# Kernel optimization log

Measured on AMD Instinct MI355X. Metric: run time of the kernel, lower is better.

## Reference

```python
import jax, jax.numpy as jnp
import numpy as np

NUM_RELATION = 7

def setup_inputs() -> dict:
    key = jax.random.key(0)
    ks = jax.random.split(key, 12)
    N, E, D, DO, R, DE = 20000, 640000, 512, 512, NUM_RELATION, 59
    inp = {
        "node_feat": jax.random.normal(ks[0], (N, D), dtype=jnp.float32),
        "edge_weight": jax.random.uniform(ks[1], (E,), dtype=jnp.float32),
        "edge_feat": jax.random.normal(ks[2], (E, DE), dtype=jnp.float32),
        "W_lin": jax.random.normal(ks[3], (DO, R * D), dtype=jnp.float32) * 0.02,
        "b_lin": jax.random.normal(ks[4], (DO,), dtype=jnp.float32) * 0.02,
        "W_self": jax.random.normal(ks[5], (DO, D), dtype=jnp.float32) * 0.02,
        "b_self": jax.random.normal(ks[6], (DO,), dtype=jnp.float32) * 0.02,
        "W_edge": jax.random.normal(ks[7], (DO, DE), dtype=jnp.float32) * 0.02,
        "b_edge": jax.random.normal(ks[8], (DO,), dtype=jnp.float32) * 0.02,
        "node_in": jax.random.randint(ks[9], (E,), 0, N, dtype=jnp.int64) if jax.config.jax_enable_x64 else jax.random.randint(ks[9], (E,), 0, N).astype(jnp.int32),
        "node_out": jax.random.randint(ks[10], (E,), 0, N).astype(jnp.int32),
        "relation": jax.random.randint(ks[11], (E,), 0, R).astype(jnp.int32),
    }
    inp["node_in"] = inp["node_in"].astype(jnp.int32)
    return inp


def reference(node_feat, edge_weight, edge_feat, W_lin, b_lin, W_self, b_self,
              W_edge, b_edge, node_in, node_out, relation):
    N, D = node_feat.shape
    R = NUM_RELATION
    # segment id: node_out * R + relation  (column index in sparse (N, N*R) adjacency)
    seg = node_out * R + relation  # [E]
    # update = adjacency.T @ input  == scatter-add of weighted source features
    msg = node_feat[node_in] * edge_weight[:, None]               # [E, D]
    update = jax.ops.segment_sum(msg, seg, num_segments=N * R)    # [N*R, D]
    # edge_linear path: edge_update scattered with the same segment ids
    edge_msg = (edge_feat @ W_edge.T + b_edge) * edge_weight[:, None]  # [E, D]
    update = update + jax.ops.segment_sum(edge_msg, seg, num_segments=N * R)
    update = update.reshape(N, R * D)                             # [N, R*D]
    # combine: linear(update) + self_loop(input), then relu
    out = update @ W_lin.T + b_lin + node_feat @ W_self.T + b_self
    return jax.nn.relu(out)
```

## Files before the change

kernel.cpp:

```cpp
#include <hip/hip_runtime.h>
#include <stdint.h>

typedef unsigned short u16;
typedef __attribute__((ext_vector_type(8))) __bf16 bf16x8;
typedef __attribute__((ext_vector_type(8))) unsigned short u16x8;
typedef __attribute__((ext_vector_type(4))) float f32x4;

#define NREL 7
#define DIM  512
#define DEDGE 59
#define KC   420
#define KCP  448
#define KTOT 4544

__device__ __forceinline__ float bf2f(u16 u) {
  union { unsigned u; float f; } c; c.u = ((unsigned)u) << 16; return c.f;
}
__device__ __forceinline__ u16 f2bf(float f) {
  union { float f; unsigned u; } c; c.f = f;
  unsigned r = ((c.u >> 16) & 1u) + 0x7FFFu;
  return (u16)((c.u + r) >> 16);
}

__device__ __forceinline__ void gload16(const void* g, void* l) {
  __builtin_amdgcn_global_load_lds(
      (__attribute__((address_space(1))) void*)g,
      (__attribute__((address_space(3))) void*)l, 16, 0, 0);
}

__global__ void convA(const float* __restrict__ in, u16* __restrict__ out, int total4) {
  int i = blockIdx.x * 256 + threadIdx.x;
  if (i >= total4) return;
  float4 v = ((const float4*)in)[i];
  ushort4 r;
  r.x = f2bf(v.x); r.y = f2bf(v.y); r.z = f2bf(v.z); r.w = f2bf(v.w);
  ((ushort4*)out)[i] = r;
}

__global__ void buildBW(const float* __restrict__ W_lin, const float* __restrict__ W_self,
                        u16* __restrict__ Bfull, int total4) {
  int gid = blockIdx.x * 256 + threadIdx.x;
  if (gid >= total4) return;
  int idx = gid * 4;
  int o = idx >> 12;
  int k = idx & 4095;
  const float* src = (k < NREL * DIM) ? (W_lin + (size_t)o * (NREL * DIM) + k)
                                      : (W_self + (size_t)o * DIM + (k - NREL * DIM));
  float4 v = *(const float4*)src;
  ushort4 rr;
  rr.x = f2bf(v.x); rr.y = f2bf(v.y); rr.z = f2bf(v.z); rr.w = f2bf(v.w);
  *(ushort4*)(Bfull + (size_t)o * KTOT + k) = rr;
}

__global__ __launch_bounds__(512) void buildCx(const float* __restrict__ W_edge,
                                               const float* __restrict__ b_edge,
                                               const float* __restrict__ W_lin,
                                               u16* __restrict__ Bfull) {
  int c = blockIdx.x;
  int o = threadIdx.x;
  u16* dst = Bfull + (size_t)o * KTOT + NREL * DIM + DIM;
  if (c >= KC) { dst[c] = 0; return; }
  __shared__ float col[DIM];
  int r;
  if (c < NREL * DEDGE) {
    r = c / DEDGE;
    int de = c - r * DEDGE;
    col[o] = W_edge[(size_t)o * DEDGE + de];
  } else {
    r = c - NREL * DEDGE;
    col[o] = b_edge[o];
  }
  __syncthreads();
  const float* wrow = W_lin + (size_t)o * (NREL * DIM) + (size_t)r * DIM;
  float acc = 0.f;
#pragma unroll 8
  for (int d = 0; d < DIM; ++d) acc += col[d] * wrow[d];
  dst[c] = f2bf(acc);
}

__global__ void countK2(const int* __restrict__ node_out, const int* __restrict__ relation,
                        int* __restrict__ counts2, int E) {
  int e = blockIdx.x * 256 + threadIdx.x;
  if (e < E) atomicAdd(&counts2[node_out[e] * 8 + relation[e]], 1);
}

__global__ void baseK(const int* __restrict__ counts2, int* __restrict__ offs2,
                      int* __restrict__ cursor2, int* __restrict__ totalCtr, int N) {
  int n = blockIdx.x * 256 + threadIdx.x;
  if (n >= N) return;
  int cnt[NREL];
  int s = 0;
#pragma unroll
  for (int r = 0; r < NREL; ++r) { cnt[r] = counts2[n * 8 + r]; s += cnt[r]; }
  int base = atomicAdd(totalCtr, s);
#pragma unroll
  for (int r = 0; r < NREL; ++r) {
    offs2[n * 8 + r] = base;
    cursor2[n * 8 + r] = base;
    base += cnt[r];
  }
  offs2[n * 8 + 7] = base;
}

__global__ void fillK2(const int* __restrict__ node_in, const int* __restrict__ node_out,
                       const int* __restrict__ relation, const float* __restrict__ ew,
                       int* __restrict__ cursor2, uint4* __restrict__ quads, int E) {
  int e = blockIdx.x * 256 + threadIdx.x;
  if (e >= E) return;
  int p = atomicAdd(&cursor2[node_out[e] * 8 + relation[e]], 1);
  quads[p] = make_uint4((unsigned)node_in[e], __float_as_uint(ew[e]), (unsigned)e, 0u);
}

__global__ __launch_bounds__(64) void gatherG2(const float* __restrict__ ef,
                                               const uint4* __restrict__ quads,
                                               const int* __restrict__ offs2,
                                               u16* __restrict__ Mfull) {
  int n = blockIdx.x;
  int lane = threadIdx.x;
  u16* row = Mfull + (size_t)n * KTOT + NREL * DIM + DIM;
  int base = n * 8;
  for (int r = 0; r < NREL; ++r) {
    int p0 = offs2[base + r], p1 = offs2[base + r + 1];
    float acc = 0.f;
    for (int p = p0; p < p1; ++p) {
      uint4 q = quads[p];
      int e = __builtin_amdgcn_readfirstlane((int)q.z);
      float w = __uint_as_float(__builtin_amdgcn_readfirstlane(q.y));
      float v = (lane < DEDGE) ? ef[(size_t)e * DEDGE + lane] : 1.0f;
      acc += w * v;
    }
    if (lane < DEDGE) row[r * DEDGE + lane] = f2bf(acc);
    else if (lane == DEDGE) row[NREL * DEDGE + r] = f2bf(acc);
  }
  if (lane >= 60) {
    for (int c = KC + (lane - 60); c < KCP; c += 4) row[c] = 0;
  }
}

__global__ __launch_bounds__(256) void aggK(const u16* __restrict__ NF,
                                            const uint4* __restrict__ quads,
                                            const int* __restrict__ offs2,
                                            u16* __restrict__ Mfull) {
  int n = blockIdx.x;
  int wid = threadIdx.x >> 6, lane = threadIdx.x & 63;
  int o0 = lane * 8;
  u16* mrow = Mfull + (size_t)n * KTOT;
  if (wid == 3) {
    *(u16x8*)(mrow + NREL * DIM + o0) = *(const u16x8*)(NF + (size_t)n * DIM + o0);
  }
  int base = n * 8;
  for (int r = wid; r < NREL; r += 4) {
    int p0 = offs2[base + r], p1 = offs2[base + r + 1];
    float a[8];
#pragma unroll
    for (int j = 0; j < 8; ++j) a[j] = 0.f;
    for (int p = p0; p < p1; ++p) {
      uint4 q = quads[p];
      int src = __builtin_amdgcn_readfirstlane((int)q.x);
      float w = __uint_as_float(__builtin_amdgcn_readfirstlane(q.y));
      u16x8 hv = *(const u16x8*)(NF + (size_t)src * DIM + o0);
#pragma unroll
      for (int j = 0; j < 8; ++j) a[j] += w * bf2f(hv[j]);
    }
    u16x8 st;
#pragma unroll
    for (int j = 0; j < 8; ++j) st[j] = f2bf(a[j]);
    *(u16x8*)(mrow + r * DIM + o0) = st;
  }
}

__global__ __launch_bounds__(256) void gemm_br(const u16* __restrict__ A,
                                               const u16* __restrict__ Bt,
                                               const float* __restrict__ b_lin,
                                               const float* __restrict__ b_self,
                                               float* __restrict__ Cout, int M) {
  __shared__ __align__(16) u16 sA[3][128 * 32];
  __shared__ __align__(16) u16 sB[3][128 * 32];
  const int tid = threadIdx.x;
  const int w = tid >> 6, l = tid & 63;
  const int lr = l & 15, kg = l >> 4;
  const int sl = kg ^ ((lr >> 1) & 3);

  const int id = blockIdx.x;
  const int npan = gridDim.x >> 2;
  const int nfull = (npan >> 3) << 3;
  int p, c;
  if (id < nfull * 4) {
    int g = id >> 5, r = id & 31;
    p = g * 8 + (r & 7);
    c = r >> 3;
  } else {
    int t = id - nfull * 4;
    p = nfull + (t >> 2);
    c = t & 3;
  }
  const int m0 = p * 128, n0 = c * 128;
  const int wr = w >> 1, wc = w & 1;
  f32x4 acc[4][4];
  const f32x4 z4 = {0.f, 0.f, 0.f, 0.f};
#pragma unroll
  for (int i = 0; i < 4; ++i)
#pragma unroll
    for (int j = 0; j < 4; ++j) acc[i][j] = z4;

  const int ktiles = KTOT / 32;

  auto stage = [&](int kt, int b) {
    const int k0 = kt * 32;
#pragma unroll
    for (int t = 0; t < 2; ++t) {
      int idx = w * 128 + t * 64 + l;
      int row = idx >> 2, kp = idx & 3;
      int s = kp ^ ((row >> 1) & 3);
      int gm = m0 + row; gm = gm < M ? gm : M - 1;
      gload16(A + (size_t)gm * KTOT + k0 + s * 8,
              (char*)sA[b] + (size_t)idx * 16);
    }
#pragma unroll
    for (int t = 0; t < 2; ++t) {
      int idx = w * 128 + t * 64 + l;
      int row = idx >> 2, kp = idx & 3;
      int s = kp ^ ((row >> 1) & 3);
      gload16(Bt + (size_t)(n0 + row) * KTOT + k0 + s * 8,
              (char*)sB[b] + (size_t)idx * 16);
    }
  };

  stage(0, 0);
  stage(1, 1);
  asm volatile("s_waitcnt vmcnt(4)" ::: "memory");
  __builtin_amdgcn_s_barrier();
  __builtin_amdgcn_sched_barrier(0);

  for (int kt = 0; kt < ktiles; ++kt) {
    const int cur = kt % 3;
    if (kt + 2 < ktiles) stage(kt + 2, (kt + 2) % 3);
    bf16x8 af[4], bfr[4];
#pragma unroll
    for (int i = 0; i < 4; ++i)
      af[i] = *(const bf16x8*)(sA[cur] + (size_t)(wr * 64 + i * 16 + lr) * 32 + sl * 8);
#pragma unroll
    for (int j = 0; j < 4; ++j)
      bfr[j] = *(const bf16x8*)(sB[cur] + (size_t)(wc * 64 + j * 16 + lr) * 32 + sl * 8);
#pragma unroll
    for (int i = 0; i < 4; ++i)
#pragma unroll
      for (int j = 0; j < 4; ++j)
        acc[i][j] = __builtin_amdgcn_mfma_f32_16x16x32_bf16(af[i], bfr[j], acc[i][j], 0, 0, 0);
    if (kt + 2 < ktiles) {
      asm volatile("s_waitcnt vmcnt(4)" ::: "memory");
    } else {
      asm volatile("s_waitcnt vmcnt(0)" ::: "memory");
    }
    __builtin_amdgcn_s_barrier();
    __builtin_amdgcn_sched_barrier(0);
  }
#pragma unroll
  for (int i = 0; i < 4; ++i) {
#pragma unroll
    for (int j = 0; j < 4; ++j) {
      int gj = n0 + wc * 64 + j * 16 + lr;
      float bias = b_lin[gj] + b_self[gj];
#pragma unroll
      for (int v = 0; v < 4; ++v) {
        int gm = m0 + wr * 64 + i * 16 + kg * 4 + v;
        if (gm < M)
          ((float*)Cout)[(size_t)gm * DIM + gj] = fmaxf(acc[i][j][v] + bias, 0.f);
      }
    }
  }
}

extern "C" void kernel_launch(void* const* d_in, const int* in_sizes, int n_in,
                              void* d_out, int out_size, void* d_ws, size_t ws_size,
                              hipStream_t stream) {
  const float* node_feat = (const float*)d_in[0];
  const float* edge_weight = (const float*)d_in[1];
  const float* edge_feat = (const float*)d_in[2];
  const float* W_lin = (const float*)d_in[3];
  const float* b_lin = (const float*)d_in[4];
  const float* W_self = (const float*)d_in[5];
  const float* b_self = (const float*)d_in[6];
  const float* W_edge = (const float*)d_in[7];
  const float* b_edge = (const float*)d_in[8];
  const int* node_in = (const int*)d_in[9];
  const int* node_out = (const int*)d_in[10];
  const int* relation = (const int*)d_in[11];
  float* out = (float*)d_out;

  const int N = in_sizes[0] / DIM;
  const int E = in_sizes[1];

  char* ws = (char*)d_ws;
  size_t off = 0;
  auto take = [&](size_t b) {
    char* p = ws + off;
    off += (b + 255) & ~(size_t)255;
    return p;
  };
  u16* NF       = (u16*)take((size_t)N * DIM * 2);
  u16* Bfull    = (u16*)take((size_t)DIM * KTOT * 2);
  u16* Mfull    = (u16*)take((size_t)N * KTOT * 2);
  int* counts2  = (int*)take((size_t)N * 8 * 4);
  int* offs2    = (int*)take((size_t)N * 8 * 4);
  int* cursor2  = (int*)take((size_t)N * 8 * 4);
  int* totalCtr = (int*)take(256);
  uint4* quads  = (uint4*)take((size_t)E * 16);
  if (off > ws_size) return;

  hipMemsetAsync(counts2, 0, (size_t)N * 8 * 4, stream);
  hipMemsetAsync(totalCtr, 0, 256, stream);

  {
    int total4 = N * DIM / 4;
    convA<<<(total4 + 255) / 256, 256, 0, stream>>>(node_feat, NF, total4);
  }
  {
    int total4 = DIM * 4096 / 4;
    buildBW<<<(total4 + 255) / 256, 256, 0, stream>>>(W_lin, W_self, Bfull, total4);
  }
  buildCx<<<KCP, 512, 0, stream>>>(W_edge, b_edge, W_lin, Bfull);

  countK2<<<(E + 255) / 256, 256, 0, stream>>>(node_out, relation, counts2, E);
  baseK<<<(N + 255) / 256, 256, 0, stream>>>(counts2, offs2, cursor2, totalCtr, N);
  fillK2<<<(E + 255) / 256, 256, 0, stream>>>(node_in, node_out, relation, edge_weight,
                                              cursor2, quads, E);

  gatherG2<<<N, 64, 0, stream>>>(edge_feat, quads, offs2, Mfull);
  aggK<<<N, 256, 0, stream>>>(NF, quads, offs2, Mfull);

  {
    int npan = (N + 127) / 128;
    gemm_br<<<npan * 4, 256, 0, stream>>>(Mfull, Bfull, b_lin, b_self, out, N);
  }
}
```

Baseline: 490.3 us.

## Fuse edge-feature gather into node aggregation and split GEMM A operand buffers

Folds the separate edge-feature gather kernel into the aggregation kernel, so each wave walks the edge list once and accumulates both node-feature and edge-feature sums. It also stops copying node_feat into a combined A matrix: the GEMM now selects among three source buffers (U, NF, G) per k-tile. A one-ahead prefetch of the next edge quad is added to the inner loop. This removes one kernel launch, a second pass over the edge indices, and the self-feature copy, at the cost of extra per-lane loads and a branch in the GEMM staging.

```diff
diff --git a/kernel.cpp b/kernel.cpp
--- a/kernel.cpp
+++ b/kernel.cpp
@@ -11,6 +11,7 @@
 #define DEDGE 59
 #define KC   420
 #define KCP  448
+#define KU   3584
 #define KTOT 4544
 
 __device__ __forceinline__ float bf2f(u16 u) {
@@ -44,8 +45,8 @@
   int idx = gid * 4;
   int o = idx >> 12;
   int k = idx & 4095;
-  const float* src = (k < NREL * DIM) ? (W_lin + (size_t)o * (NREL * DIM) + k)
-                                      : (W_self + (size_t)o * DIM + (k - NREL * DIM));
+  const float* src = (k < KU) ? (W_lin + (size_t)o * KU + k)
+                              : (W_self + (size_t)o * DIM + (k - KU));
   float4 v = *(const float4*)src;
   ushort4 rr;
   rr.x = f2bf(v.x); rr.y = f2bf(v.y); rr.z = f2bf(v.z); rr.w = f2bf(v.w);
@@ -58,7 +59,7 @@
                                                u16* __restrict__ Bfull) {
   int c = blockIdx.x;
   int o = threadIdx.x;
-  u16* dst = Bfull + (size_t)o * KTOT + NREL * DIM + DIM;
+  u16* dst = Bfull + (size_t)o * KTOT + KU + DIM;
   if (c >= KC) { dst[c] = 0; return; }
   __shared__ float col[DIM];
   int r;
@@ -71,7 +72,7 @@
     col[o] = b_edge[o];
   }
   __syncthreads();
-  const float* wrow = W_lin + (size_t)o * (NREL * DIM) + (size_t)r * DIM;
+  const float* wrow = W_lin + (size_t)o * KU + (size_t)r * DIM;
   float acc = 0.f;
 #pragma unroll 8
   for (int d = 0; d < DIM; ++d) acc += col[d] * wrow[d];
@@ -111,65 +112,52 @@
   quads[p] = make_uint4((unsigned)node_in[e], __float_as_uint(ew[e]), (unsigned)e, 0u);
 }
 
-__global__ __launch_bounds__(64) void gatherG2(const float* __restrict__ ef,
-                                               const uint4* __restrict__ quads,
-                                               const int* __restrict__ offs2,
-                                               u16* __restrict__ Mfull) {
-  int n = blockIdx.x;
-  int lane = threadIdx.x;
-  u16* row = Mfull + (size_t)n * KTOT + NREL * DIM + DIM;
-  int base = n * 8;
-  for (int r = 0; r < NREL; ++r) {
-    int p0 = offs2[base + r], p1 = offs2[base + r + 1];
-    float acc = 0.f;
-    for (int p = p0; p < p1; ++p) {
-      uint4 q = quads[p];
-      int e = __builtin_amdgcn_readfirstlane((int)q.z);
-      float w = __uint_as_float(__builtin_amdgcn_readfirstlane(q.y));
-      float v = (lane < DEDGE) ? ef[(size_t)e * DEDGE + lane] : 1.0f;
-      acc += w * v;
-    }
-    if (lane < DEDGE) row[r * DEDGE + lane] = f2bf(acc);
-    else if (lane == DEDGE) row[NREL * DEDGE + r] = f2bf(acc);
-  }
-  if (lane >= 60) {
-    for (int c = KC + (lane - 60); c < KCP; c += 4) row[c] = 0;
-  }
-}
-
 __global__ __launch_bounds__(256) void aggK(const u16* __restrict__ NF,
+                                            const float* __restrict__ ef,
                                             const uint4* __restrict__ quads,
                                             const int* __restrict__ offs2,
-                                            u16* __restrict__ Mfull) {
+                                            u16* __restrict__ U,
+                                            u16* __restrict__ G) {
   int n = blockIdx.x;
   int wid = threadIdx.x >> 6, lane = threadIdx.x & 63;
   int o0 = lane * 8;
-  u16* mrow = Mfull + (size_t)n * KTOT;
-  if (wid == 3) {
-    *(u16x8*)(mrow + NREL * DIM + o0) = *(const u16x8*)(NF + (size_t)n * DIM + o0);
-  }
+  u16* urow = U + (size_t)n * KU;
+  u16* grow = G + (size_t)n * KCP;
+  if (wid == 3 && lane < KCP - KC) grow[KC + lane] = 0;
   int base = n * 8;
   for (int r = wid; r < NREL; r += 4) {
     int p0 = offs2[base + r], p1 = offs2[base + r + 1];
     float a[8];
 #pragma unroll
     for (int j = 0; j < 8; ++j) a[j] = 0.f;
-    for (int p = p0; p < p1; ++p) {
-      uint4 q = quads[p];
-      int src = __builtin_amdgcn_readfirstlane((int)q.x);
-      float w = __uint_as_float(__builtin_amdgcn_readfirstlane(q.y));
-      u16x8 hv = *(const u16x8*)(NF + (size_t)src * DIM + o0);
-#pragma unroll
-      for (int j = 0; j < 8; ++j) a[j] += w * bf2f(hv[j]);
+    float ag = 0.f;
+    if (p0 < p1) {
+      uint4 q = quads[p0];
+      for (int p = p0; p < p1; ++p) {
+        uint4 qn = (p + 1 < p1) ? quads[p + 1] : q;
+        int src = __builtin_amdgcn_readfirstlane((int)q.x);
+        float w = __uint_as_float(__builtin_amdgcn_readfirstlane(q.y));
+        int e = __builtin_amdgcn_readfirstlane((int)q.z);
+        u16x8 hv = *(const u16x8*)(NF + (size_t)src * DIM + o0);
+        float vef = (lane < DEDGE) ? ef[(size_t)e * DEDGE + lane] : 1.0f;
+#pragma unroll
+        for (int j = 0; j < 8; ++j) a[j] += w * bf2f(hv[j]);
+        ag += w * vef;
+        q = qn;
+      }
     }
     u16x8 st;
 #pragma unroll
     for (int j = 0; j < 8; ++j) st[j] = f2bf(a[j]);
-    *(u16x8*)(mrow + r * DIM + o0) = st;
-  }
-}
-
-__global__ __launch_bounds__(256) void gemm_br(const u16* __restrict__ A,
+    *(u16x8*)(urow + (size_t)r * DIM + o0) = st;
+    if (lane < DEDGE) grow[r * DEDGE + lane] = f2bf(ag);
+    else if (lane == DEDGE) grow[NREL * DEDGE + r] = f2bf(ag);
+  }
+}
+
+__global__ __launch_bounds__(256) void gemm_br(const u16* __restrict__ U,
+                                               const u16* __restrict__ NF,
+                                               const u16* __restrict__ G,
                                                const u16* __restrict__ Bt,
                                                const float* __restrict__ b_lin,
                                                const float* __restrict__ b_self,
@@ -206,6 +194,10 @@
   const int ktiles = KTOT / 32;
 
   auto stage = [&](int kt, int b) {
+    const u16* Ab; int astr, ac0;
+    if (kt < 112)      { Ab = U;  astr = KU;  ac0 = kt * 32; }
+    else if (kt < 128) { Ab = NF; astr = DIM; ac0 = kt * 32 - KU; }
+    else               { Ab = G;  astr = KCP; ac0 = kt * 32 - (KU + DIM); }
     const int k0 = kt * 32;
 #pragma unroll
     for (int t = 0; t < 2; ++t) {
@@ -213,7 +205,7 @@
       int row = idx >> 2, kp = idx & 3;
       int s = kp ^ ((row >> 1) & 3);
       int gm = m0 + row; gm = gm < M ? gm : M - 1;
-      gload16(A + (size_t)gm * KTOT + k0 + s * 8,
+      gload16(Ab + (size_t)gm * astr + ac0 + s * 8,
               (char*)sA[b] + (size_t)idx * 16);
     }
 #pragma unroll
@@ -300,7 +292,8 @@
   };
   u16* NF       = (u16*)take((size_t)N * DIM * 2);
   u16* Bfull    = (u16*)take((size_t)DIM * KTOT * 2);
-  u16* Mfull    = (u16*)take((size_t)N * KTOT * 2);
+  u16* U        = (u16*)take((size_t)N * KU * 2);
+  u16* G        = (u16*)take((size_t)N * KCP * 2);
   int* counts2  = (int*)take((size_t)N * 8 * 4);
   int* offs2    = (int*)take((size_t)N * 8 * 4);
   int* cursor2  = (int*)take((size_t)N * 8 * 4);
@@ -326,11 +319,10 @@
   fillK2<<<(E + 255) / 256, 256, 0, stream>>>(node_in, node_out, relation, edge_weight,
                                               cursor2, quads, E);
 
-  gatherG2<<<N, 64, 0, stream>>>(edge_feat, quads, offs2, Mfull);
-  aggK<<<N, 256, 0, stream>>>(NF, quads, offs2, Mfull);
+  aggK<<<N, 256, 0, stream>>>(NF, edge_feat, quads, offs2, U, G);
 
   {
     int npan = (N + 127) / 128;
-    gemm_br<<<npan * 4, 256, 0, stream>>>(Mfull, Bfull, b_lin, b_self, out, N);
-  }
-}
+    gemm_br<<<npan * 4, 256, 0, stream>>>(U, NF, G, Bfull, b_lin, b_self, out, N);
+  }
+}
```

After: 547.7 us. +11.7%, slower.
